# Kernel optimization log

Hardware: AMD Instinct MI355X
Metric: run time of the kernel (lower is better)

## Reference

```python
import jax, jax.numpy as jnp
import numpy as np

B, S, E, H = 2, 2048, 1024, 16
D = E // H  # head_dim = 64


def setup_inputs() -> dict:
    key = jax.random.key(0)
    ks = jax.random.split(key, 5)
    return {
        "hidden_states": jax.random.normal(ks[0], (B, S, E), jnp.float32),
        "c_attn_w": jax.random.normal(ks[1], (E, 3 * E), jnp.float32) * 0.02,
        "c_attn_b": jnp.zeros((3 * E,), jnp.float32),
        "c_proj_w": jax.random.normal(ks[2], (E, E), jnp.float32) * 0.02,
        "c_proj_b": jnp.zeros((E,), jnp.float32),
    }


def reference(hidden_states, c_attn_w, c_attn_b, c_proj_w, c_proj_b):
    # Conv1D: x @ w + b -> qkv [B, S, 3E]
    qkv = hidden_states @ c_attn_w + c_attn_b
    q, k, v = jnp.split(qkv, 3, axis=-1)
    # [B, H, S, D]
    q = q.reshape(B, S, H, D).transpose(0, 2, 1, 3)
    k = k.reshape(B, S, H, D).transpose(0, 2, 1, 3)
    v = v.reshape(B, S, H, D).transpose(0, 2, 1, 3)
    # scores [B, H, S, S], scaled by sqrt(head_dim)
    scores = jnp.einsum("bhqd,bhkd->bhqk", q, k) / jnp.sqrt(jnp.asarray(D, q.dtype))
    causal = jnp.tril(jnp.ones((S, S), bool))  # [S, S]
    mask_value = jnp.finfo(scores.dtype).min
    scores = jnp.where(causal, scores, mask_value)
    attn = jax.nn.softmax(scores, axis=-1)
    # attn @ V -> [B, H, S, D] -> [B, S, E]
    out = jnp.einsum("bhqk,bhkd->bhqd", attn, v)
    out = out.transpose(0, 2, 1, 3).reshape(B, S, E)
    return out @ c_proj_w + c_proj_b
```

## Files before the change

### kernel.cpp

```cpp
#include <hip/hip_runtime.h>

using bf16 = __bf16;
typedef __bf16 bf16x8 __attribute__((ext_vector_type(8)));
typedef __bf16 bf16x4 __attribute__((ext_vector_type(4)));
typedef float  f32x4  __attribute__((ext_vector_type(4)));

#define MFMA16(a, b, c) __builtin_amdgcn_mfma_f32_16x16x32_bf16((a), (b), (c), 0, 0, 0)
#define VMW(n) asm volatile("s_waitcnt vmcnt(" #n ")" ::: "memory")

static constexpr int S = 2048, E = 1024;
static constexpr float CSCALE = 0.18033688011112042f;

__device__ __forceinline__ void gld16(const bf16* g, bf16* l) {
    __builtin_amdgcn_global_load_lds((const __attribute__((address_space(1))) unsigned*)g,
                                     (__attribute__((address_space(3))) unsigned*)l, 16, 0, 0);
}

__device__ __forceinline__ void gload4(const bf16* p, bf16x8& r0, bf16x8& r1, bf16x8& r2, bf16x8& r3) {
    asm volatile("global_load_dwordx4 %0, %4, off\n\t"
                 "global_load_dwordx4 %1, %4, off offset:1024\n\t"
                 "global_load_dwordx4 %2, %4, off offset:2048\n\t"
                 "global_load_dwordx4 %3, %4, off offset:3072"
                 : "=&v"(r0), "=&v"(r1), "=&v"(r2), "=&v"(r3)
                 : "v"(p));
}

__global__ __launch_bounds__(256) void k_prep(const float* __restrict__ hs, const float* __restrict__ w0,
                                              const float* __restrict__ w1, bf16* __restrict__ A0,
                                              bf16* __restrict__ Wt0, bf16* __restrict__ Wt1) {
    __shared__ float tile[32][33];
    const int bx = blockIdx.x;
    if (bx < 4096) {
        int i = (bx * 256 + threadIdx.x) * 4;
        float4 v = *(const float4*)(hs + i);
        bf16x4 o = { (bf16)v.x, (bf16)v.y, (bf16)v.z, (bf16)v.w };
        *(bf16x4*)(A0 + i) = o;
        return;
    }
    const float* in;
    bf16* outp;
    int K, N, nb, kb;
    bool frag;
    if (bx < 4096 + 3072) {
        int j = bx - 4096; in = w0; outp = Wt0; K = 1024; N = 3072; nb = j % 96; kb = j / 96; frag = true;
    } else {
        int j = bx - 7168; in = w1; outp = Wt1; K = 1024; N = 1024; nb = j % 32; kb = j / 32; frag = false;
    }
    const int bxx = nb * 32, byy = kb * 32;
    const int tx = threadIdx.x & 31, ty = threadIdx.x >> 5;
#pragma unroll
    for (int i = 0; i < 32; i += 8)
        tile[ty + i][tx] = in[(long)(byy + ty + i) * N + bxx + tx];
    __syncthreads();
    if (frag) {
        if (threadIdx.x < 128) {
            const int nl = threadIdx.x >> 2;
            const int kq = threadIdx.x & 3;
            const int n = bxx + nl, k = byy + kq * 8;
            bf16x8 v;
#pragma unroll
            for (int e = 0; e < 8; ++e) v[e] = (bf16)tile[kq * 8 + e][nl];
            const long addr = (((long)(n >> 6) * 32 + (k >> 5)) * 4 + ((n >> 4) & 3)) * 512
                            + ((k >> 3) & 3) * 128 + (n & 15) * 8;
            *(bf16x8*)(outp + addr) = v;
        }
    } else {
#pragma unroll
        for (int i = 0; i < 32; i += 8)
            outp[(long)(bxx + ty + i) * K + byy + tx] = (bf16)tile[tx][ty + i];
    }
}

__global__ __launch_bounds__(384, 3) void k_gemm_qkv(const bf16* __restrict__ A, const bf16* __restrict__ Bt,
                                                     const float* __restrict__ bias, bf16* __restrict__ Qs,
                                                     bf16* __restrict__ Kf, bf16* __restrict__ Vf, int Kk) {
    __shared__ __align__(16) char smem[28672];
    bf16* sA = (bf16*)smem;

    const int NT = Kk >> 5;

    const int bid = blockIdx.x;
    const int sid = (bid & 7) * 64 + (bid >> 3);
    const long bm = (long)(sid & 31) * 128;
    const long bn = (long)(sid >> 5) * 192;

    const int tid = threadIdx.x;
    const int w = tid >> 6, lane = tid & 63;
    const int col = lane & 15, quad = lane >> 4;
    const int wc = w % 3, wr = w / 3;
    const int wrow = wr * 64, wcol = wc * 64;

    const int u0 = w * 64 + lane;
    const int r0s = u0 >> 2, kq0 = u0 & 3;
    const bf16* gA0 = A + (bm + r0s) * Kk + ((kq0 ^ ((r0s >> 1) & 3)) * 8);
    const int u1 = 384 + ((w & 1) * 64) + lane;
    const int r1s = u1 >> 2, kq1 = u1 & 3;
    const bf16* gA1 = A + (bm + r1s) * Kk + ((kq1 ^ ((r1s >> 1) & 3)) * 8);

    const int strip = (int)(sid >> 5) * 3 + wc;
    const bf16* wfb = Bt + (long)strip * 65536 + lane * 8;

    f32x4 acc[4][4] = {};
    bf16x8 b00, b01, b02, b03, b10, b11, b12, b13;

    gld16(gA0, sA + u0 * 8);
    if (w < 2) gld16(gA1, sA + u1 * 8);
    gld16(gA0 + 32, sA + 4096 + u0 * 8);
    if (w < 2) gld16(gA1 + 32, sA + 4096 + u1 * 8);
    gload4(wfb, b00, b01, b02, b03);
    gload4(wfb + 2048, b10, b11, b12, b13);
    VMW(8);
    __builtin_amdgcn_s_barrier();
    __builtin_amdgcn_sched_barrier(0);

#define QSTEP(T, B0, B1, B2, B3, BWL, BWH, AWL, AWH) do {                                 \
    const int t_ = (T);                                                                   \
    const bf16* sAs = sA + (t_ % 3) * 4096;                                               \
    bf16x8 af0, af1, af2, af3;                                                            \
    { const int r_ = wrow + col;      af0 = *(const bf16x8*)(sAs + r_ * 32 + ((quad ^ ((r_ >> 1) & 3)) * 8)); } \
    { const int r_ = wrow + 16 + col; af1 = *(const bf16x8*)(sAs + r_ * 32 + ((quad ^ ((r_ >> 1) & 3)) * 8)); } \
    { const int r_ = wrow + 32 + col; af2 = *(const bf16x8*)(sAs + r_ * 32 + ((quad ^ ((r_ >> 1) & 3)) * 8)); } \
    { const int r_ = wrow + 48 + col; af3 = *(const bf16x8*)(sAs + r_ * 32 + ((quad ^ ((r_ >> 1) & 3)) * 8)); } \
    const bool pf_ = (t_ + 2 < NT);                                                       \
    if (pf_) {                                                                            \
        bf16* dA = sA + ((t_ + 2) % 3) * 4096;                                            \
        gld16(gA0 + (t_ + 2) * 32, dA + u0 * 8);                                          \
        if (w < 2) gld16(gA1 + (t_ + 2) * 32, dA + u1 * 8);                               \
    }                                                                                     \
    if (w < 2) VMW(BWL); else VMW(BWH);                                                   \
    __builtin_amdgcn_sched_barrier(0);                                                    \
    __builtin_amdgcn_s_setprio(1);                                                        \
    acc[0][0] = MFMA16(af0, B0, acc[0][0]); acc[0][1] = MFMA16(af0, B1, acc[0][1]);       \
    acc[0][2] = MFMA16(af0, B2, acc[0][2]); acc[0][3] = MFMA16(af0, B3, acc[0][3]);       \
    acc[1][0] = MFMA16(af1, B0, acc[1][0]); acc[1][1] = MFMA16(af1, B1, acc[1][1]);       \
    acc[1][2] = MFMA16(af1, B2, acc[1][2]); acc[1][3] = MFMA16(af1, B3, acc[1][3]);       \
    acc[2][0] = MFMA16(af2, B0, acc[2][0]); acc[2][1] = MFMA16(af2, B1, acc[2][1]);       \
    acc[2][2] = MFMA16(af2, B2, acc[2][2]); acc[2][3] = MFMA16(af2, B3, acc[2][3]);       \
    acc[3][0] = MFMA16(af3, B0, acc[3][0]); acc[3][1] = MFMA16(af3, B1, acc[3][1]);       \
    acc[3][2] = MFMA16(af3, B2, acc[3][2]); acc[3][3] = MFMA16(af3, B3, acc[3][3]);       \
    __builtin_amdgcn_s_setprio(0);                                                        \
    if (pf_) gload4(wfb + (long)(t_ + 2) * 2048, B0, B1, B2, B3);                         \
    if (w < 2) VMW(AWL); else VMW(AWH);                                                   \
    __builtin_amdgcn_s_barrier();                                                         \
    __builtin_amdgcn_sched_barrier(0);                                                    \
} while (0)

    QSTEP(0, b00, b01, b02, b03, 6, 5, 10, 9);
    QSTEP(1, b10, b11, b12, b13, 8, 6, 10, 9);
#pragma unroll 1
    for (int t = 2; t + 2 < NT; t += 2) {
        QSTEP(t,     b00, b01, b02, b03, 8, 6, 10, 9);
        QSTEP(t + 1, b10, b11, b12, b13, 8, 6, 10, 9);
    }
    QSTEP(NT - 2, b00, b01, b02, b03, 0, 0, 0, 0);
    QSTEP(NT - 1, b10, b11, b12, b13, 0, 0, 0, 0);
#undef QSTEP

    const long gc0 = bn + wcol;
    const int seg = (int)(gc0 >> 10);
    float bv[4];
#pragma unroll
    for (int nt = 0; nt < 4; ++nt) bv[nt] = bias[gc0 + nt * 16 + col];

    if (seg == 0) {
#pragma unroll
        for (int nt = 0; nt < 4; ++nt) {
            const long gc = gc0 + nt * 16 + col;
#pragma unroll
            for (int mt = 0; mt < 4; ++mt) {
                const long gr = bm + wrow + mt * 16 + quad * 4;
#pragma unroll
                for (int r = 0; r < 4; ++r)
                    Qs[(gr + r) * 1024 + gc] = (bf16)((acc[mt][nt][r] + bv[nt]) * CSCALE);
            }
        }
        return;
    }

    bf16* myT = (bf16*)smem + w * 2304;
    const int bmi = (int)bm;
    const int b = bmi >> 11;
    const int ktw = ((bmi & 2047) >> 6) + wr;
    const int head = (int)((gc0 & 1023) >> 6);
    const int bh = b * 16 + head;

    if (seg == 1) {
#pragma unroll
        for (int h = 0; h < 2; ++h) {
#pragma unroll
            for (int mt = 0; mt < 4; ++mt)
#pragma unroll
                for (int nt2 = 0; nt2 < 2; ++nt2) {
                    const int nt = 2 * h + nt2;
#pragma unroll
                    for (int r = 0; r < 4; ++r)
                        myT[(mt * 16 + quad * 4 + r) * 36 + nt2 * 16 + col] =
                            (bf16)(acc[mt][nt][r] + bv[nt]);
                }
#pragma unroll
            for (int mtp = 0; mtp < 4; ++mtp) {
                bf16x8 ch = *(const bf16x8*)(myT + (mtp * 16 + col) * 36 + quad * 8);
                const long chunk = ((long)(bh * 32 + ktw) * 8 + mtp * 2 + h) * 64 + lane;
                *(bf16x8*)(Kf + chunk * 8) = ch;
            }
        }
    } else {
#pragma unroll
        for (int h = 0; h < 2; ++h) {
#pragma unroll
            for (int nt2 = 0; nt2 < 2; ++nt2) {
                const int nt = 2 * h + nt2;
#pragma unroll
                for (int mt = 0; mt < 4; ++mt) {
                    bf16x4 pk = { (bf16)(acc[mt][nt][0] + bv[nt]), (bf16)(acc[mt][nt][1] + bv[nt]),
                                  (bf16)(acc[mt][nt][2] + bv[nt]), (bf16)(acc[mt][nt][3] + bv[nt]) };
                    *(bf16x4*)(myT + (nt2 * 16 + col) * 72 + mt * 16 + quad * 4) = pk;
                }
            }
#pragma unroll
            for (int dt2 = 0; dt2 < 2; ++dt2) {
                const int dt = 2 * h + dt2;
#pragma unroll
                for (int ks = 0; ks < 2; ++ks) {
                    bf16x8 ch = *(const bf16x8*)(myT + (dt2 * 16 + col) * 72 + ks * 32 + quad * 8);
                    const long chunk = ((long)(bh * 32 + ktw) * 8 + dt * 2 + ks) * 64 + lane;
                    *(bf16x8*)(Vf + chunk * 8) = ch;
                }
            }
        }
    }
}

__global__ __launch_bounds__(256) void k_gemm_bt64(const bf16* __restrict__ A, const bf16* __restrict__ Bt,
                                                    const float* __restrict__ bias, float* __restrict__ Cout,
                                                    int Mm, int Nn, int Kk) {
    const int bm = blockIdx.x * 64;
    const int bn = blockIdx.y * 128;
    const int tid = threadIdx.x;
    const int w = tid >> 6, lane = tid & 63;
    const int wm = (w >> 1) * 32, wn = (w & 1) * 64;
    const int col = lane & 15, quad = lane >> 4;

    __shared__ bf16 sA[64 * 64];
    __shared__ bf16 sB[128 * 64];

    const bf16* pA[2]; bf16* lA[2];
#pragma unroll
    for (int i = 0; i < 2; i++) {
        const int c = i * 256 + w * 64 + lane;
        const int r = c >> 3, sl = (c & 7) ^ (r & 7);
        pA[i] = A + (long)(bm + r) * Kk + sl * 8;
        lA[i] = sA + i * 2048 + w * 512;
    }
    const bf16* pB[4]; bf16* lB[4];
#pragma unroll
    for (int i = 0; i < 4; i++) {
        const int c = i * 256 + w * 64 + lane;
        const int r = c >> 3, sl = (c & 7) ^ (r & 7);
        pB[i] = Bt + (long)(bn + r) * Kk + sl * 8;
        lB[i] = sB + i * 2048 + w * 512;
    }

    f32x4 acc[2][4] = {};

    for (int k0 = 0; k0 < Kk; k0 += 64) {
        __syncthreads();
#pragma unroll
        for (int i = 0; i < 2; i++) gld16(pA[i] + k0, lA[i]);
#pragma unroll
        for (int i = 0; i < 4; i++) gld16(pB[i] + k0, lB[i]);
        __syncthreads();
#pragma unroll
        for (int h = 0; h < 2; h++) {
            bf16x8 af[2], bfr[4];
#pragma unroll
            for (int mt = 0; mt < 2; mt++) {
                const int row = wm + mt * 16 + col;
                af[mt] = *(const bf16x8*)(sA + row * 64 + (((h * 4 + quad) ^ (col & 7)) * 8));
            }
#pragma unroll
            for (int nt = 0; nt < 4; nt++) {
                const int row = wn + nt * 16 + col;
                bfr[nt] = *(const bf16x8*)(sB + row * 64 + (((h * 4 + quad) ^ (col & 7)) * 8));
            }
#pragma unroll
            for (int mt = 0; mt < 2; mt++)
#pragma unroll
                for (int nt = 0; nt < 4; nt++)
                    acc[mt][nt] = MFMA16(af[mt], bfr[nt], acc[mt][nt]);
        }
    }

#pragma unroll
    for (int mt = 0; mt < 2; mt++) {
        const int gr = bm + wm + mt * 16 + quad * 4;
#pragma unroll
        for (int nt = 0; nt < 4; nt++) {
            const int gc = bn + wn + nt * 16 + col;
            const float bv = bias[gc];
#pragma unroll
            for (int r = 0; r < 4; r++)
                Cout[(long)(gr + r) * Nn + gc] = acc[mt][nt][r] + bv;
        }
    }
}

__global__ __launch_bounds__(128) void k_attn(const bf16* __restrict__ Qs, const bf16* __restrict__ Kf,
                                              const bf16* __restrict__ Vf, bf16* __restrict__ out) {
    const int bh = blockIdx.x & 31;
    const int t = 63 - (blockIdx.x >> 5);
    const int b = bh >> 4, h = bh & 15;
    const int tid = threadIdx.x;
    const int w = tid >> 6, lane = tid & 63;
    const int col = lane & 15, quad = lane >> 4;

    __shared__ bf16 sP[2][32 * 72];
    __shared__ float M[64][36];
    bf16* pw = sP[w];

    const bf16* kfb = Kf + ((long)bh << 17) + lane * 8;
    const bf16* vfb = Vf + ((long)bh << 17) + lane * 8;

    const int q0 = t * 32;
    const int nkt = (t >> 1) + 1;
    const int kA = nkt >> 1;
    const int kbeg = w ? kA : 0;
    const int kend = w ? nkt : kA;

    bf16x8 bq[2][2];
#pragma unroll
    for (int qg = 0; qg < 2; qg++) {
        const bf16* qp = Qs + (long)(b * S + q0 + qg * 16 + col) * E + h * 64 + quad * 8;
        bq[qg][0] = *(const bf16x8*)(qp);
        bq[qg][1] = *(const bf16x8*)(qp + 32);
    }
    float m_[2] = { -1e30f, -1e30f }, l_[2] = { 0.f, 0.f };
    f32x4 o[2][4] = {};

#pragma unroll 1
    for (int kt = kbeg; kt < kend; kt++) {
        bf16x8 kfr[4][2], vfr[4][2];
#pragma unroll
        for (int mt = 0; mt < 4; mt++)
#pragma unroll
            for (int half = 0; half < 2; half++)
                kfr[mt][half] = *(const bf16x8*)(kfb + ((long)(kt * 8 + mt * 2 + half) << 9));
#pragma unroll
        for (int dt = 0; dt < 4; dt++)
#pragma unroll
            for (int ks = 0; ks < 2; ks++)
                vfr[dt][ks] = *(const bf16x8*)(vfb + ((long)(kt * 8 + dt * 2 + ks) << 9));

        f32x4 s[2][4];
#pragma unroll
        for (int mt = 0; mt < 4; mt++)
#pragma unroll
            for (int qg = 0; qg < 2; qg++) {
                f32x4 z = {};
                z = MFMA16(kfr[mt][0], bq[qg][0], z);
                z = MFMA16(kfr[mt][1], bq[qg][1], z);
                s[qg][mt] = z;
            }
        if (kt == nkt - 1) {
#pragma unroll
            for (int qg = 0; qg < 2; qg++) {
                const int qrow = q0 + qg * 16 + col;
#pragma unroll
                for (int mt = 0; mt < 4; mt++)
#pragma unroll
                    for (int r = 0; r < 4; r++)
                        if (kt * 64 + mt * 16 + quad * 4 + r > qrow) s[qg][mt][r] = -1e30f;
            }
        }
#pragma unroll
        for (int qg = 0; qg < 2; qg++) {
            float cm = -1e30f;
#pragma unroll
            for (int mt = 0; mt < 4; mt++)
#pragma unroll
                for (int r = 0; r < 4; r++) cm = fmaxf(cm, s[qg][mt][r]);
            cm = fmaxf(cm, __shfl_xor(cm, 16));
            cm = fmaxf(cm, __shfl_xor(cm, 32));
            const float mnew = fmaxf(m_[qg], cm);
            const float alpha = __builtin_amdgcn_exp2f(m_[qg] - mnew);
            m_[qg] = mnew;
            float rs = 0.f;
#pragma unroll
            for (int mt = 0; mt < 4; mt++)
#pragma unroll
                for (int r = 0; r < 4; r++) {
                    float pe = __builtin_amdgcn_exp2f(s[qg][mt][r] - mnew);
                    s[qg][mt][r] = pe;
                    rs += pe;
                }
            l_[qg] = l_[qg] * alpha + rs;
#pragma unroll
            for (int dt = 0; dt < 4; dt++)
#pragma unroll
                for (int r = 0; r < 4; r++) o[qg][dt][r] *= alpha;
#pragma unroll
            for (int mt = 0; mt < 4; mt++) {
                bf16x4 pk = { (bf16)s[qg][mt][0], (bf16)s[qg][mt][1],
                              (bf16)s[qg][mt][2], (bf16)s[qg][mt][3] };
                *(bf16x4*)(pw + (qg * 16 + col) * 72 + mt * 16 + quad * 4) = pk;
            }
        }
#pragma unroll
        for (int ks = 0; ks < 2; ks++) {
            bf16x8 ap[2];
#pragma unroll
            for (int qg = 0; qg < 2; qg++)
                ap[qg] = *(const bf16x8*)(pw + (qg * 16 + col) * 72 + ks * 32 + quad * 8);
#pragma unroll
            for (int dt = 0; dt < 4; dt++)
#pragma unroll
                for (int qg = 0; qg < 2; qg++)
                    o[qg][dt] = MFMA16(vfr[dt][ks], ap[qg], o[qg][dt]);
        }
    }

#pragma unroll
    for (int qg = 0; qg < 2; qg++) {
        float lt = l_[qg];
        lt += __shfl_xor(lt, 16);
        lt += __shfl_xor(lt, 32);
        l_[qg] = lt;
    }

    if (w == 0) {
#pragma unroll
        for (int qg = 0; qg < 2; qg++) {
#pragma unroll
            for (int dt = 0; dt < 4; dt++)
                *(f32x4*)&M[lane][qg * 16 + dt * 4] = o[qg][dt];
            M[lane][32 + qg * 2] = m_[qg];
            M[lane][33 + qg * 2] = l_[qg];
        }
    }
    __syncthreads();
    if (w == 1) {
#pragma unroll
        for (int qg = 0; qg < 2; qg++) {
            const float m0 = M[lane][32 + qg * 2];
            const float l0 = M[lane][33 + qg * 2];
            const float mm = fmaxf(m0, m_[qg]);
            const float a0 = __builtin_amdgcn_exp2f(m0 - mm);
            const float a1 = __builtin_amdgcn_exp2f(m_[qg] - mm);
            const float li = 1.f / (l0 * a0 + l_[qg] * a1);
            bf16* op = out + (long)(b * S + q0 + qg * 16 + col) * E + h * 64 + quad * 4;
#pragma unroll
            for (int dt = 0; dt < 4; dt++) {
                f32x4 o0 = *(const f32x4*)&M[lane][qg * 16 + dt * 4];
                bf16x4 ov;
#pragma unroll
                for (int r = 0; r < 4; r++)
                    ov[r] = (bf16)((o0[r] * a0 + o[qg][dt][r] * a1) * li);
                *(bf16x4*)(op + dt * 16) = ov;
            }
        }
    }
}

extern "C" void kernel_launch(void* const* d_in, const int* in_sizes, int n_in,
                              void* d_out, int out_size, void* d_ws, size_t ws_size,
                              hipStream_t stream) {
    const float* hs = (const float*)d_in[0];
    const float* w0 = (const float*)d_in[1];
    const float* b0 = (const float*)d_in[2];
    const float* w1 = (const float*)d_in[3];
    const float* b1 = (const float*)d_in[4];
    float* outp = (float*)d_out;

    char* ws = (char*)d_ws;
    bf16* A0    = (bf16*)(ws);
    bf16* Wt0   = (bf16*)(ws + 8388608);
    bf16* Wt1   = (bf16*)(ws + 14680064);
    bf16* Qs    = (bf16*)(ws + 16777216);
    bf16* Kf    = (bf16*)(ws + 25165824);
    bf16* Vf    = (bf16*)(ws + 33554432);
    bf16* attnO = (bf16*)(ws + 41943040);

    k_prep<<<8192, 256, 0, stream>>>(hs, w0, w1, A0, Wt0, Wt1);
    k_gemm_qkv<<<512, 384, 0, stream>>>(A0, Wt0, b0, Qs, Kf, Vf, 1024);
    k_attn<<<2048, 128, 0, stream>>>(Qs, Kf, Vf, attnO);
    k_gemm_bt64<<<dim3(64, 8), 256, 0, stream>>>(attnO, Wt1, b1, outp, 4096, 1024, 1024);
}
```

Measured before the change: 176.1 us.

## Split attention KV range across four waves with a 4-way softmax merge

The attention kernel now splits each query tile's key range across four wavefronts instead of two, with a 256-thread block. Three waves write their partial O, max and sum to shared memory, and the fourth merges all four with log-sum-exp rescaling. This adds intra-block parallelism so short causal rows finish sooner and latency is hidden better. In exchange it uses more shared memory and does a heavier merge step, and small tiles leave some waves with no key tiles to process.

```diff
diff --git a/kernel.cpp b/kernel.cpp
--- a/kernel.cpp
+++ b/kernel.cpp
@@ -305,7 +305,7 @@
     }
 }
 
-__global__ __launch_bounds__(128) void k_attn(const bf16* __restrict__ Qs, const bf16* __restrict__ Kf,
+__global__ __launch_bounds__(256) void k_attn(const bf16* __restrict__ Qs, const bf16* __restrict__ Kf,
                                               const bf16* __restrict__ Vf, bf16* __restrict__ out) {
     const int bh = blockIdx.x & 31;
     const int t = 63 - (blockIdx.x >> 5);
@@ -314,8 +314,8 @@
     const int w = tid >> 6, lane = tid & 63;
     const int col = lane & 15, quad = lane >> 4;
 
-    __shared__ bf16 sP[2][32 * 72];
-    __shared__ float M[64][36];
+    __shared__ bf16 sP[4][32 * 72];
+    __shared__ float M[3][64][36];
     bf16* pw = sP[w];
 
     const bf16* kfb = Kf + ((long)bh << 17) + lane * 8;
@@ -323,9 +323,8 @@
 
     const int q0 = t * 32;
     const int nkt = (t >> 1) + 1;
-    const int kA = nkt >> 1;
-    const int kbeg = w ? kA : 0;
-    const int kend = w ? nkt : kA;
+    const int kbeg = (w * nkt) >> 2;
+    const int kend = ((w + 1) * nkt) >> 2;
 
     bf16x8 bq[2][2];
 #pragma unroll
@@ -427,34 +426,47 @@
         l_[qg] = lt;
     }
 
-    if (w == 0) {
+    if (w < 3) {
 #pragma unroll
         for (int qg = 0; qg < 2; qg++) {
 #pragma unroll
             for (int dt = 0; dt < 4; dt++)
-                *(f32x4*)&M[lane][qg * 16 + dt * 4] = o[qg][dt];
-            M[lane][32 + qg * 2] = m_[qg];
-            M[lane][33 + qg * 2] = l_[qg];
+                *(f32x4*)&M[w][lane][qg * 16 + dt * 4] = o[qg][dt];
+            M[w][lane][32 + qg * 2] = m_[qg];
+            M[w][lane][33 + qg * 2] = l_[qg];
         }
     }
     __syncthreads();
-    if (w == 1) {
+    if (w == 3) {
 #pragma unroll
         for (int qg = 0; qg < 2; qg++) {
-            const float m0 = M[lane][32 + qg * 2];
-            const float l0 = M[lane][33 + qg * 2];
-            const float mm = fmaxf(m0, m_[qg]);
-            const float a0 = __builtin_amdgcn_exp2f(m0 - mm);
-            const float a1 = __builtin_amdgcn_exp2f(m_[qg] - mm);
-            const float li = 1.f / (l0 * a0 + l_[qg] * a1);
+            float mm = m_[qg];
+#pragma unroll
+            for (int i = 0; i < 3; i++) mm = fmaxf(mm, M[i][lane][32 + qg * 2]);
+            const float a3 = __builtin_amdgcn_exp2f(m_[qg] - mm);
+            float ai[3];
+            float lsum = l_[qg] * a3;
+#pragma unroll
+            for (int i = 0; i < 3; i++) {
+                ai[i] = __builtin_amdgcn_exp2f(M[i][lane][32 + qg * 2] - mm);
+                lsum += ai[i] * M[i][lane][33 + qg * 2];
+            }
+            const float li = 1.f / lsum;
             bf16* op = out + (long)(b * S + q0 + qg * 16 + col) * E + h * 64 + quad * 4;
 #pragma unroll
             for (int dt = 0; dt < 4; dt++) {
-                f32x4 o0 = *(const f32x4*)&M[lane][qg * 16 + dt * 4];
+                f32x4 oa;
+#pragma unroll
+                for (int r = 0; r < 4; r++) oa[r] = o[qg][dt][r] * a3;
+#pragma unroll
+                for (int i = 0; i < 3; i++) {
+                    f32x4 oi = *(const f32x4*)&M[i][lane][qg * 16 + dt * 4];
+#pragma unroll
+                    for (int r = 0; r < 4; r++) oa[r] += oi[r] * ai[i];
+                }
                 bf16x4 ov;
 #pragma unroll
-                for (int r = 0; r < 4; r++)
-                    ov[r] = (bf16)((o0[r] * a0 + o[qg][dt][r] * a1) * li);
+                for (int r = 0; r < 4; r++) ov[r] = (bf16)(oa[r] * li);
                 *(bf16x4*)(op + dt * 16) = ov;
             }
         }
@@ -482,6 +494,6 @@
 
     k_prep<<<8192, 256, 0, stream>>>(hs, w0, w1, A0, Wt0, Wt1);
     k_gemm_qkv<<<512, 384, 0, stream>>>(A0, Wt0, b0, Qs, Kf, Vf, 1024);
-    k_attn<<<2048, 128, 0, stream>>>(Qs, Kf, Vf, attnO);
+    k_attn<<<2048, 256, 0, stream>>>(Qs, Kf, Vf, attnO);
     k_gemm_bt64<<<dim3(64, 8), 256, 0, stream>>>(attnO, Wt1, b1, outp, 4096, 1024, 1024);
 }
```

Measured after the change: 179.2 us. Within noise of the previous version (+1.8%).
